# Kernel optimization log

Hardware: AMD Instinct MI355X
Metric: run time of the kernel (lower is better)

## Reference

```python
import jax, jax.numpy as jnp
import numpy as np

MAX_DISP = 4  # pad_size == max_displacement per module validation
EPS = 1e-12   # torch F.normalize default eps


def _l2_normalize(x):
    # F.normalize(x) with default dim=1 (channels), p=2
    norm = jnp.sqrt(jnp.sum(x * x, axis=1, keepdims=True))
    return x / jnp.maximum(norm, EPS)


def setup_inputs() -> dict:
    key = jax.random.key(0)
    k1, k2 = jax.random.split(key)
    B, C, H, W = 8, 256, 96, 128
    fr = jax.random.normal(k1, (B, C, H, W), dtype=jnp.float32)
    fq = jax.random.normal(k2, (B, C, H, W), dtype=jnp.float32)
    return {"fr": fr, "fq": fq}


def reference(fr, fq):
    r = MAX_DISP
    H, W = fr.shape[2], fr.shape[3]
    frn = _l2_normalize(fr)
    # Normalization is per-pixel over channels, so normalize-then-pad equals
    # pad-then-normalize (padded zero columns stay zero under the eps clamp).
    fq_pad = jnp.pad(_l2_normalize(fq), ((0, 0), (0, 0), (r, r), (r, r)))
    # Offset order: dy (rows) outer, dx (cols) inner -> matches torch meshgrid 'ij' flatten.
    outs = [
        jnp.mean(frn * fq_pad[:, :, dy:H + dy, dx:W + dx], axis=1, keepdims=True)
        for dy in range(2 * r + 1)
        for dx in range(2 * r + 1)
    ]
    return jnp.concatenate(outs, axis=1)  # (B, (2r+1)^2, H, W)
```

## Files before the change

### kernel.cpp

```cpp
#include <hip/hip_runtime.h>


#define BB 8
#define CC 256
#define HH 96
#define WW 128
#define HW (HH*WW)
#define CHW (CC*HW)
#define NDISP 81
#define TYS 4
#define GD 3
#define HROWS (TYS+GD-1)
#define HX4 18
#define NSLOT (HROWS*HX4)
#define CK 4
#define CKHW (CK*HW)
#define NCHK (CC/CK)
#define NST (NSLOT*CK)
#define YT (HH/TYS)
#define XT 2
#define NTILES (BB*YT*XT)
#define NGRP 3
#define EPSN 1e-12f

__device__ __forceinline__ void dma16(const void* g, void* l) {
    __builtin_amdgcn_global_load_lds(
        (const __attribute__((address_space(1))) void*)g,
        (__attribute__((address_space(3))) void*)l,
        16, 0, 0);
}

__global__ __launch_bounds__(64) __attribute__((amdgpu_waves_per_eu(2, 8)))
void corr_kernel(
    const float* __restrict__ fr, const float* __restrict__ fq,
    float* __restrict__ out)
{
    __shared__ float4 s_fq[2][NST];

    const int lane = threadIdx.x;
    const int tx   = lane & 15;
    const int ty   = lane >> 4;

    const int tile = blockIdx.x % NTILES;
    const int dyg  = blockIdx.x / NTILES;
    const int b    = tile / (YT * XT);
    const int rem  = tile % (YT * XT);
    const int y0   = (rem >> 1) * TYS;
    const int x0   = (rem & 1) * 64;

    int soff[7];
#pragma unroll
    for (int j = 0; j < 7; ++j) {
        int i = 64 * j + lane;
        int c    = (i / NSLOT) & 3;
        int s    = i % NSLOT;
        int row  = s / HX4;
        int col4 = s % HX4;
        int gy = y0 + 3 * dyg - 4 + row;
        int gx = x0 - 4 + col4 * 4;
        gy = min(max(gy, 0), HH - 1);
        gx = min(max(gx, 0), WW - 4);
        soff[j] = b * CHW + c * HW + gy * WW + gx;
    }

    const int frbase = b * CHW + (y0 + ty) * WW + x0 + tx * 4;

#pragma unroll
    for (int j = 0; j < 6; ++j)
        dma16(fq + soff[j], &s_fq[0][64 * j]);
    if (lane < 48)
        dma16(fq + soff[6], &s_fq[0][384]);

    float4 fra[CK];
#pragma unroll
    for (int c = 0; c < CK; ++c)
        fra[c] = *(const float4*)(fr + frbase + c * HW);

    float4 acc[GD][9];
#pragma unroll
    for (int g = 0; g < GD; ++g)
#pragma unroll
        for (int d = 0; d < 9; ++d) acc[g][d] = make_float4(0.f, 0.f, 0.f, 0.f);
    float sqn[GD][12];
#pragma unroll
    for (int g = 0; g < GD; ++g)
#pragma unroll
        for (int i = 0; i < 12; ++i) sqn[g][i] = 0.f;
    float4 fr2 = make_float4(0.f, 0.f, 0.f, 0.f);

#pragma unroll 1
    for (int ch = 0; ch < NCHK; ++ch) {
        const int p   = ch & 1;
        const int nch = (ch + 1 < NCHK) ? ch + 1 : ch;
        const int nco = nch * CKHW;

#pragma unroll
        for (int j = 0; j < 6; ++j)
            dma16(fq + soff[j] + nco, &s_fq[1 - p][64 * j]);
        if (lane < 48)
            dma16(fq + soff[6] + nco, &s_fq[1 - p][384]);

        __builtin_amdgcn_s_waitcnt(0x0F7B);
        __builtin_amdgcn_sched_barrier(0);

#pragma unroll
        for (int c = 0; c < CK; ++c) {
            float4 a = fra[c];
            fra[c] = *(const float4*)(fr + frbase + nco + c * HW);
            fr2.x += a.x * a.x; fr2.y += a.y * a.y;
            fr2.z += a.z * a.z; fr2.w += a.w * a.w;

#pragma unroll
            for (int g = 0; g < GD; ++g) {
                float rw[12];
#pragma unroll
                for (int s4 = 0; s4 < 3; ++s4) {
                    float4 t = s_fq[p][c * NSLOT + (ty + g) * HX4 + tx + s4];
                    rw[s4 * 4 + 0] = t.x;
                    rw[s4 * 4 + 1] = t.y;
                    rw[s4 * 4 + 2] = t.z;
                    rw[s4 * 4 + 3] = t.w;
                }
#pragma unroll
                for (int i = 0; i < 12; ++i) sqn[g][i] += rw[i] * rw[i];
#pragma unroll
                for (int dx = 0; dx < 9; ++dx) {
                    acc[g][dx].x += a.x * rw[dx + 0];
                    acc[g][dx].y += a.y * rw[dx + 1];
                    acc[g][dx].z += a.z * rw[dx + 2];
                    acc[g][dx].w += a.w * rw[dx + 3];
                }
            }
        }
    }

    __builtin_amdgcn_s_waitcnt(0x0F70);

    float4 ir;
    ir.x = 1.0f / fmaxf(sqrtf(fr2.x), EPSN);
    ir.y = 1.0f / fmaxf(sqrtf(fr2.y), EPSN);
    ir.z = 1.0f / fmaxf(sqrtf(fr2.z), EPSN);
    ir.w = 1.0f / fmaxf(sqrtf(fr2.w), EPSN);

    const int  xe0   = x0 + tx * 4;
    const float inv256 = 1.0f / 256.0f;

#pragma unroll
    for (int g = 0; g < GD; ++g) {
        const int dy = 3 * dyg + g;
        float inq[12];
#pragma unroll
        for (int i = 0; i < 12; ++i)
            inq[i] = 1.0f / fmaxf(sqrtf(sqn[g][i]), EPSN);

        const bool rowok = ((unsigned)(y0 + ty + dy - 4) < (unsigned)HH);
        const int obase = (b * NDISP + dy * 9) * HW + (y0 + ty) * WW + xe0;
#pragma unroll
        for (int dx = 0; dx < 9; ++dx) {
            float4 a = acc[g][dx];
            float4 o;
            o.x = a.x * ir.x * inq[dx + 0] * inv256;
            o.y = a.y * ir.y * inq[dx + 1] * inv256;
            o.z = a.z * ir.z * inq[dx + 2] * inv256;
            o.w = a.w * ir.w * inq[dx + 3] * inv256;
            const int cb = xe0 + dx - 4;
            o.x = (rowok && (unsigned)(cb    ) < (unsigned)WW) ? o.x : 0.f;
            o.y = (rowok && (unsigned)(cb + 1) < (unsigned)WW) ? o.y : 0.f;
            o.z = (rowok && (unsigned)(cb + 2) < (unsigned)WW) ? o.z : 0.f;
            o.w = (rowok && (unsigned)(cb + 3) < (unsigned)WW) ? o.w : 0.f;
            *(float4*)(out + obase + dx * HW) = o;
        }
    }
}

extern "C" void kernel_launch(void* const* d_in, const int* in_sizes, int n_in,
                              void* d_out, int out_size, void* d_ws, size_t ws_size,
                              hipStream_t stream) {
    const float* fr = (const float*)d_in[0];
    const float* fq = (const float*)d_in[1];
    float* out = (float*)d_out;
    corr_kernel<<<dim3(NTILES * NGRP), dim3(64), 0, stream>>>(fr, fq, out);
}
```

Baseline: 284.8 us.

## Split channel reduction across two waves per block with LDS reduction

Measured after the change: 296.2 us. +4.0%, slower.

```diff
diff --git a/kernel.cpp b/kernel.cpp
--- a/kernel.cpp
+++ b/kernel.cpp
@@ -15,7 +15,8 @@
 #define NSLOT (HROWS*HX4)
 #define CK 4
 #define CKHW (CK*HW)
-#define NCHK (CC/CK)
+#define NW 2
+#define NCHW (CC/(CK*NW))
 #define NST (NSLOT*CK)
 #define YT (HH/TYS)
 #define XT 2
@@ -30,14 +31,15 @@
         16, 0, 0);
 }
 
-__global__ __launch_bounds__(64) __attribute__((amdgpu_waves_per_eu(2, 8)))
+__global__ __launch_bounds__(128) __attribute__((amdgpu_waves_per_eu(2, 8)))
 void corr_kernel(
     const float* __restrict__ fr, const float* __restrict__ fq,
     float* __restrict__ out)
 {
-    __shared__ float4 s_fq[2][NST];
-
-    const int lane = threadIdx.x;
+    __shared__ float4 s_fq[NW][2][NST];
+
+    const int lane = threadIdx.x & 63;
+    const int wid  = threadIdx.x >> 6;
     const int tx   = lane & 15;
     const int ty   = lane >> 4;
 
@@ -47,6 +49,8 @@
     const int rem  = tile % (YT * XT);
     const int y0   = (rem >> 1) * TYS;
     const int x0   = (rem & 1) * 64;
+
+    const int cbase = wid * (NCHW * CKHW);
 
     int soff[7];
 #pragma unroll
@@ -60,16 +64,16 @@
         int gx = x0 - 4 + col4 * 4;
         gy = min(max(gy, 0), HH - 1);
         gx = min(max(gx, 0), WW - 4);
-        soff[j] = b * CHW + c * HW + gy * WW + gx;
-    }
-
-    const int frbase = b * CHW + (y0 + ty) * WW + x0 + tx * 4;
+        soff[j] = b * CHW + cbase + c * HW + gy * WW + gx;
+    }
+
+    const int frbase = b * CHW + cbase + (y0 + ty) * WW + x0 + tx * 4;
 
 #pragma unroll
     for (int j = 0; j < 6; ++j)
-        dma16(fq + soff[j], &s_fq[0][64 * j]);
+        dma16(fq + soff[j], &s_fq[wid][0][64 * j]);
     if (lane < 48)
-        dma16(fq + soff[6], &s_fq[0][384]);
+        dma16(fq + soff[6], &s_fq[wid][0][384]);
 
     float4 fra[CK];
 #pragma unroll
@@ -89,16 +93,16 @@
     float4 fr2 = make_float4(0.f, 0.f, 0.f, 0.f);
 
 #pragma unroll 1
-    for (int ch = 0; ch < NCHK; ++ch) {
+    for (int ch = 0; ch < NCHW; ++ch) {
         const int p   = ch & 1;
-        const int nch = (ch + 1 < NCHK) ? ch + 1 : ch;
+        const int nch = (ch + 1 < NCHW) ? ch + 1 : ch;
         const int nco = nch * CKHW;
 
 #pragma unroll
         for (int j = 0; j < 6; ++j)
-            dma16(fq + soff[j] + nco, &s_fq[1 - p][64 * j]);
+            dma16(fq + soff[j] + nco, &s_fq[wid][1 - p][64 * j]);
         if (lane < 48)
-            dma16(fq + soff[6] + nco, &s_fq[1 - p][384]);
+            dma16(fq + soff[6] + nco, &s_fq[wid][1 - p][384]);
 
         __builtin_amdgcn_s_waitcnt(0x0F7B);
         __builtin_amdgcn_sched_barrier(0);
@@ -115,7 +119,7 @@
                 float rw[12];
 #pragma unroll
                 for (int s4 = 0; s4 < 3; ++s4) {
-                    float4 t = s_fq[p][c * NSLOT + (ty + g) * HX4 + tx + s4];
+                    float4 t = s_fq[wid][p][c * NSLOT + (ty + g) * HX4 + tx + s4];
                     rw[s4 * 4 + 0] = t.x;
                     rw[s4 * 4 + 1] = t.y;
                     rw[s4 * 4 + 2] = t.z;
@@ -135,6 +139,52 @@
     }
 
     __builtin_amdgcn_s_waitcnt(0x0F70);
+
+    float4* red = &s_fq[0][0][0];
+    __syncthreads();
+    if (wid) {
+#pragma unroll
+        for (int g = 0; g < GD; ++g)
+#pragma unroll
+            for (int d = 0; d < 9; ++d)
+                red[lane * 27 + g * 9 + d] = acc[g][d];
+    }
+    __syncthreads();
+    if (!wid) {
+#pragma unroll
+        for (int g = 0; g < GD; ++g)
+#pragma unroll
+            for (int d = 0; d < 9; ++d) {
+                float4 t = red[lane * 27 + g * 9 + d];
+                acc[g][d].x += t.x; acc[g][d].y += t.y;
+                acc[g][d].z += t.z; acc[g][d].w += t.w;
+            }
+    }
+    __syncthreads();
+    if (wid) {
+#pragma unroll
+        for (int g = 0; g < GD; ++g)
+#pragma unroll
+            for (int i = 0; i < 3; ++i)
+                red[lane * 10 + g * 3 + i] = make_float4(
+                    sqn[g][4*i+0], sqn[g][4*i+1], sqn[g][4*i+2], sqn[g][4*i+3]);
+        red[lane * 10 + 9] = fr2;
+    }
+    __syncthreads();
+    if (wid) return;
+
+#pragma unroll
+    for (int g = 0; g < GD; ++g)
+#pragma unroll
+        for (int i = 0; i < 3; ++i) {
+            float4 t = red[lane * 10 + g * 3 + i];
+            sqn[g][4*i+0] += t.x; sqn[g][4*i+1] += t.y;
+            sqn[g][4*i+2] += t.z; sqn[g][4*i+3] += t.w;
+        }
+    {
+        float4 t = red[lane * 10 + 9];
+        fr2.x += t.x; fr2.y += t.y; fr2.z += t.z; fr2.w += t.w;
+    }
 
     float4 ir;
     ir.x = 1.0f / fmaxf(sqrtf(fr2.x), EPSN);
@@ -179,5 +229,5 @@
     const float* fr = (const float*)d_in[0];
     const float* fq = (const float*)d_in[1];
     float* out = (float*)d_out;
-    corr_kernel<<<dim3(NTILES * NGRP), dim3(64), 0, stream>>>(fr, fq, out);
+    corr_kernel<<<dim3(NTILES * NGRP), dim3(128), 0, stream>>>(fr, fq, out);
 }
```
